# Kernel optimization log

Hardware: AMD Instinct MI355X
Metric: run time of the kernel (lower is better)

Reference implementation:

```python
import jax, jax.numpy as jnp
import numpy as np

H = 32  # GRU hidden size fixed by the module


def setup_inputs() -> dict:
    key = jax.random.key(0)
    ks = jax.random.split(key, 6)
    B, T, F = 4096, 60, 158
    s_ih = 1.0 / np.sqrt(H)
    return {
        "x": jax.random.normal(ks[0], (B, T, F), dtype=jnp.float32),
        "w_ih": jax.random.normal(ks[1], (3 * H, F), dtype=jnp.float32) * s_ih,
        "w_hh": jax.random.normal(ks[2], (3 * H, H), dtype=jnp.float32) * s_ih,
        "w1": jax.random.normal(ks[3], (16, H), dtype=jnp.float32) * (1.0 / np.sqrt(H)),
        "b1": jax.random.normal(ks[4], (16,), dtype=jnp.float32) * 0.01,
        "w2": jax.random.normal(ks[5], (1, 16), dtype=jnp.float32) * 0.25,
    }


def _gru_last_hidden(x, w_ih, w_hh):
    # x: [B, T, F]. Precompute input projections for all timesteps (one big GEMM),
    # then scan the sequential hidden-state recurrence over T.
    B = x.shape[0]
    gi = jnp.einsum("btf,gf->tbg", x, w_ih)  # [T, B, 3H]
    h0 = jnp.zeros((B, H), dtype=x.dtype)

    def step(h, gi_t):
        gh = h @ w_hh.T  # [B, 3H]
        i_r, i_z, i_n = jnp.split(gi_t, 3, axis=-1)
        h_r, h_z, h_n = jnp.split(gh, 3, axis=-1)
        r = jax.nn.sigmoid(i_r + h_r)
        z = jax.nn.sigmoid(i_z + h_z)
        n = jnp.tanh(i_n + r * h_n)
        h_new = (1.0 - z) * n + z * h
        return h_new, None

    h_last, _ = jax.lax.scan(step, h0, gi)
    return h_last  # [B, H]


def reference(x, w_ih, w_hh, w1, b1, w2):
    h = _gru_last_hidden(x, w_ih, w_hh)          # h_n[-1]: [B, 32]
    y = jax.nn.relu(h @ w1.T + b1)               # [B, 16]
    return y @ w2.T                              # [B, 1]
```

## Files before the change

### kernel.cpp

```cpp
#include <hip/hip_runtime.h>
#include <hip/hip_bf16.h>

#define BATCH 4096
#define TT 60
#define FF 158
#define HH 32
#define GG 96

typedef float f4 __attribute__((ext_vector_type(4), aligned(4)));
typedef float f2 __attribute__((ext_vector_type(2), aligned(4)));

__device__ __forceinline__ float fexp(float x) {
    return __builtin_amdgcn_exp2f(x * 1.442695040888963f);
}
__device__ __forceinline__ float fsigmoid(float x) {
    return __builtin_amdgcn_rcpf(1.0f + fexp(-x));
}
__device__ __forceinline__ float ftanh(float x) {
    float e = fexp(2.0f * x);
    return (e - 1.0f) * __builtin_amdgcn_rcpf(e + 1.0f);
}

__global__ __launch_bounds__(256, 2) void k1_gemm(
    const float* __restrict__ x, const float* __restrict__ w_ih,
    float* __restrict__ gs, int t0, int Tc)
{
    __shared__ float wsT[GG][161];
    __shared__ float xs[4][8][132];

    const int tid  = threadIdx.x;
    const int lane = tid & 63;
    const int wv   = tid >> 6;

    for (int i = tid; i < GG * FF; i += 256) {
        int g = i / FF;
        int k = i - g * FF;
        wsT[g][k] = w_ih[i];
    }

    const int tcol = lane & 15;
    const int trow = lane >> 4;
    const int g0   = tcol * 6;

    const int srow = lane >> 1;
    const int q    = lane & 1;
    const int Rs   = blockIdx.x * 128 + wv * 32 + srow;
    const int bs   = Rs / Tc;
    const int ts   = Rs - bs * Tc;
    const float* xrow = x + ((size_t)bs * TT + (size_t)(t0 + ts)) * FF + q * 4;

    {
        f4 p0 = *(const f4*)xrow;
        xs[wv][q * 4 + 0][srow] = p0.x;
        xs[wv][q * 4 + 1][srow] = p0.y;
        xs[wv][q * 4 + 2][srow] = p0.z;
        xs[wv][q * 4 + 3][srow] = p0.w;
    }
    __syncthreads();

    float acc[8][6];
    #pragma unroll
    for (int u = 0; u < 8; ++u)
        #pragma unroll
        for (int i = 0; i < 6; ++i) acc[u][i] = 0.0f;

    for (int s = 0; s < 19; ++s) {
        const int  k0n  = (s + 1) * 8;
        const bool tnxt = (s == 18);
        f4 pfn; f2 pf2;
        if (!tnxt) {
            pfn = *(const f4*)(xrow + k0n);
        } else {
            if (q == 0) pfn = *(const f4*)(xrow + k0n);
            else        pf2 = *(const f2*)(xrow + k0n);
        }

        const int kbase = s * 8;
        #pragma unroll
        for (int kk = 0; kk < 8; ++kk) {
            const f4 a0 = *(const f4*)&xs[wv][kk][trow * 8];
            const f4 a1 = *(const f4*)&xs[wv][kk][trow * 8 + 4];
            float bv[6];
            #pragma unroll
            for (int i = 0; i < 6; ++i) bv[i] = wsT[g0 + i][kbase + kk];
            #pragma unroll
            for (int i = 0; i < 6; ++i) {
                acc[0][i] = fmaf(a0.x, bv[i], acc[0][i]);
                acc[1][i] = fmaf(a0.y, bv[i], acc[1][i]);
                acc[2][i] = fmaf(a0.z, bv[i], acc[2][i]);
                acc[3][i] = fmaf(a0.w, bv[i], acc[3][i]);
                acc[4][i] = fmaf(a1.x, bv[i], acc[4][i]);
                acc[5][i] = fmaf(a1.y, bv[i], acc[5][i]);
                acc[6][i] = fmaf(a1.z, bv[i], acc[6][i]);
                acc[7][i] = fmaf(a1.w, bv[i], acc[7][i]);
            }
        }

        if (!tnxt) {
            xs[wv][q * 4 + 0][srow] = pfn.x;
            xs[wv][q * 4 + 1][srow] = pfn.y;
            xs[wv][q * 4 + 2][srow] = pfn.z;
            xs[wv][q * 4 + 3][srow] = pfn.w;
        } else {
            if (q == 0) {
                xs[wv][0][srow] = pfn.x;
                xs[wv][1][srow] = pfn.y;
                xs[wv][2][srow] = pfn.z;
                xs[wv][3][srow] = pfn.w;
            } else {
                xs[wv][4][srow] = pf2.x;
                xs[wv][5][srow] = pf2.y;
            }
        }
    }
    {
        #pragma unroll
        for (int kk = 0; kk < 6; ++kk) {
            const f4 a0 = *(const f4*)&xs[wv][kk][trow * 8];
            const f4 a1 = *(const f4*)&xs[wv][kk][trow * 8 + 4];
            float bv[6];
            #pragma unroll
            for (int i = 0; i < 6; ++i) bv[i] = wsT[g0 + i][152 + kk];
            #pragma unroll
            for (int i = 0; i < 6; ++i) {
                acc[0][i] = fmaf(a0.x, bv[i], acc[0][i]);
                acc[1][i] = fmaf(a0.y, bv[i], acc[1][i]);
                acc[2][i] = fmaf(a0.z, bv[i], acc[2][i]);
                acc[3][i] = fmaf(a0.w, bv[i], acc[3][i]);
                acc[4][i] = fmaf(a1.x, bv[i], acc[4][i]);
                acc[5][i] = fmaf(a1.y, bv[i], acc[5][i]);
                acc[6][i] = fmaf(a1.z, bv[i], acc[6][i]);
                acc[7][i] = fmaf(a1.w, bv[i], acc[7][i]);
            }
        }
    }

    #pragma unroll
    for (int u = 0; u < 8; ++u) {
        int R2 = blockIdx.x * 128 + wv * 32 + trow * 8 + u;
        int b2 = R2 / Tc;
        int t2 = R2 - b2 * Tc;
        float* dst = gs + ((size_t)t2 * BATCH + b2) * GG + g0;
        f2 v0 = {acc[u][0], acc[u][1]};
        f2 v1 = {acc[u][2], acc[u][3]};
        f2 v2 = {acc[u][4], acc[u][5]};
        *(f2*)(dst)     = v0;
        *(f2*)(dst + 2) = v1;
        *(f2*)(dst + 4) = v2;
    }
}

__global__ __launch_bounds__(256, 2) void k2_rec(
    const float* __restrict__ gs, const float* __restrict__ w_hh,
    float* __restrict__ hio, int Tc, int first, int last,
    const float* __restrict__ w1, const float* __restrict__ b1,
    const float* __restrict__ w2, float* __restrict__ out)
{
    __shared__ float hs[8][36];
    __shared__ float ys[8][16];
    const int tid = threadIdx.x;
    const int bl  = tid >> 5;
    const int j   = tid & 31;
    const int b   = blockIdx.x * 8 + bl;

    float wr[32], wz[32], wn[32];
    #pragma unroll
    for (int kk = 0; kk < 8; ++kk) {
        f4 a = *(const f4*)&w_hh[(size_t)(j     ) * HH + kk * 4];
        f4 c = *(const f4*)&w_hh[(size_t)(j + 32) * HH + kk * 4];
        f4 d = *(const f4*)&w_hh[(size_t)(j + 64) * HH + kk * 4];
        wr[kk*4] = a.x; wr[kk*4+1] = a.y; wr[kk*4+2] = a.z; wr[kk*4+3] = a.w;
        wz[kk*4] = c.x; wz[kk*4+1] = c.y; wz[kk*4+2] = c.z; wz[kk*4+3] = c.w;
        wn[kk*4] = d.x; wn[kk*4+1] = d.y; wn[kk*4+2] = d.z; wn[kk*4+3] = d.w;
    }

    float h = first ? 0.0f : hio[(size_t)b * HH + j];
    hs[bl][j] = h;

    const float*  gb = gs + (size_t)b * GG + j;
    const size_t  TS = (size_t)BATCH * GG;

#define K2_STEP(GIR, GIZ, GIN) {                                              \
        float gr = 0.0f, gz = 0.0f, gn = 0.0f;                                \
        _Pragma("unroll")                                                     \
        for (int k = 0; k < 32; k += 4) {                                     \
            f4 hv = *(const f4*)&hs[bl][k];                                   \
            gr = fmaf(wr[k  ], hv.x, gr); gz = fmaf(wz[k  ], hv.x, gz); gn = fmaf(wn[k  ], hv.x, gn); \
            gr = fmaf(wr[k+1], hv.y, gr); gz = fmaf(wz[k+1], hv.y, gz); gn = fmaf(wn[k+1], hv.y, gn); \
            gr = fmaf(wr[k+2], hv.z, gr); gz = fmaf(wz[k+2], hv.z, gz); gn = fmaf(wn[k+2], hv.z, gn); \
            gr = fmaf(wr[k+3], hv.w, gr); gz = fmaf(wz[k+3], hv.w, gz); gn = fmaf(wn[k+3], hv.w, gn); \
        }                                                                     \
        float r = fsigmoid((GIR) + gr);                                       \
        float z = fsigmoid((GIZ) + gz);                                       \
        float n = ftanh((GIN) + r * gn);                                      \
        h = (1.0f - z) * n + z * h;                                           \
        hs[bl][j] = h;                                                        \
    }

    float c0[18], c1[18];
    const int nfull = Tc / 6;

    if (nfull > 0) {
        #pragma unroll
        for (int u = 0; u < 6; ++u) {
            c0[u*3+0] = gb[(size_t)u * TS];
            c0[u*3+1] = gb[(size_t)u * TS + 32];
            c0[u*3+2] = gb[(size_t)u * TS + 64];
        }
    }

    int c = 0;
    while (c < nfull) {
        if (c + 1 < nfull) {
            const int tb = (c + 1) * 6;
            #pragma unroll
            for (int u = 0; u < 6; ++u) {
                c1[u*3+0] = gb[(size_t)(tb+u) * TS];
                c1[u*3+1] = gb[(size_t)(tb+u) * TS + 32];
                c1[u*3+2] = gb[(size_t)(tb+u) * TS + 64];
            }
        }
        #pragma unroll
        for (int u = 0; u < 6; ++u) K2_STEP(c0[u*3], c0[u*3+1], c0[u*3+2]);
        ++c;
        if (c >= nfull) break;

        if (c + 1 < nfull) {
            const int tb = (c + 1) * 6;
            #pragma unroll
            for (int u = 0; u < 6; ++u) {
                c0[u*3+0] = gb[(size_t)(tb+u) * TS];
                c0[u*3+1] = gb[(size_t)(tb+u) * TS + 32];
                c0[u*3+2] = gb[(size_t)(tb+u) * TS + 64];
            }
        }
        #pragma unroll
        for (int u = 0; u < 6; ++u) K2_STEP(c1[u*3], c1[u*3+1], c1[u*3+2]);
        ++c;
    }
    for (int t = nfull * 6; t < Tc; ++t) {
        float gir = gb[(size_t)t * TS];
        float giz = gb[(size_t)t * TS + 32];
        float gin = gb[(size_t)t * TS + 64];
        K2_STEP(gir, giz, gin);
    }
#undef K2_STEP

    if (last) {
        if (j < 16) {
            float y = b1[j];
            #pragma unroll
            for (int k = 0; k < 32; ++k) y = fmaf(w1[j * HH + k], hs[bl][k], y);
            ys[bl][j] = fmaxf(y, 0.0f);
        }
        if (j == 0) {
            float o = 0.0f;
            #pragma unroll
            for (int k = 0; k < 16; ++k) o = fmaf(ys[bl][k], w2[k], o);
            out[b] = o;
        }
    } else {
        hio[(size_t)b * HH + j] = h;
    }
}

extern "C" void kernel_launch(void* const* d_in, const int* in_sizes, int n_in,
                              void* d_out, int out_size, void* d_ws, size_t ws_size,
                              hipStream_t stream)
{
    const float* x    = (const float*)d_in[0];
    const float* w_ih = (const float*)d_in[1];
    const float* w_hh = (const float*)d_in[2];
    const float* w1   = (const float*)d_in[3];
    const float* b1   = (const float*)d_in[4];
    const float* w2   = (const float*)d_in[5];
    float* out = (float*)d_out;

    const size_t hbytes = (size_t)BATCH * HH * 4;
    size_t avail = (ws_size > hbytes) ? (ws_size - hbytes) : 0;
    int Tc = (int)(avail / ((size_t)BATCH * GG * 4));
    if (Tc > TT) Tc = TT;
    if (Tc < 1) Tc = 1;

    float* gsbuf = (float*)d_ws;
    float* hio   = (float*)((char*)d_ws + (size_t)BATCH * GG * 4 * (size_t)Tc);

    for (int t0 = 0; t0 < TT; ) {
        int tc = TT - t0; if (tc > Tc) tc = Tc;
        k1_gemm<<<BATCH * tc / 128, 256, 0, stream>>>(x, w_ih, gsbuf, t0, tc);
        int first = (t0 == 0) ? 1 : 0;
        int lastf = (t0 + tc >= TT) ? 1 : 0;
        k2_rec<<<BATCH / 8, 256, 0, stream>>>(gsbuf, w_hh, hio, tc, first, lastf,
                                              w1, b1, w2, out);
        t0 += tc;
    }
}
```

Before: 329.5 us.

## Halve k1 LDS footprint via two-phase weight staging; split k2 dot-product chains

Result: slower. 429.3 us (+30.3%).

```diff
diff --git a/kernel.cpp b/kernel.cpp
--- a/kernel.cpp
+++ b/kernel.cpp
@@ -21,22 +21,16 @@
     return (e - 1.0f) * __builtin_amdgcn_rcpf(e + 1.0f);
 }
 
-__global__ __launch_bounds__(256, 2) void k1_gemm(
+__global__ __launch_bounds__(256, 4) void k1_gemm(
     const float* __restrict__ x, const float* __restrict__ w_ih,
     float* __restrict__ gs, int t0, int Tc)
 {
-    __shared__ float wsT[GG][161];
-    __shared__ float xs[4][8][132];
+    __shared__ float ws[80][97];
+    __shared__ float xs[4][8][32];
 
     const int tid  = threadIdx.x;
     const int lane = tid & 63;
     const int wv   = tid >> 6;
-
-    for (int i = tid; i < GG * FF; i += 256) {
-        int g = i / FF;
-        int k = i - g * FF;
-        wsT[g][k] = w_ih[i];
-    }
 
     const int tcol = lane & 15;
     const int trow = lane >> 4;
@@ -49,6 +43,11 @@
     const int ts   = Rs - bs * Tc;
     const float* xrow = x + ((size_t)bs * TT + (size_t)(t0 + ts)) * FF + q * 4;
 
+    for (int i = tid; i < GG * 80; i += 256) {
+        int g = i / 80;
+        int k = i - g * 80;
+        ws[k][g] = w_ih[g * FF + k];
+    }
     {
         f4 p0 = *(const f4*)xrow;
         xs[wv][q * 4 + 0][srow] = p0.x;
@@ -64,43 +63,63 @@
         #pragma unroll
         for (int i = 0; i < 6; ++i) acc[u][i] = 0.0f;
 
-    for (int s = 0; s < 19; ++s) {
-        const int  k0n  = (s + 1) * 8;
-        const bool tnxt = (s == 18);
+#define K1_INNER(KL) {                                                        \
+        const f4 a0 = *(const f4*)&xs[wv][kk][trow * 8];                      \
+        const f4 a1 = *(const f4*)&xs[wv][kk][trow * 8 + 4];                  \
+        const f2 b01 = *(const f2*)&ws[KL][g0];                               \
+        const f2 b23 = *(const f2*)&ws[KL][g0 + 2];                           \
+        const f2 b45 = *(const f2*)&ws[KL][g0 + 4];                           \
+        const float bv[6] = {b01.x, b01.y, b23.x, b23.y, b45.x, b45.y};       \
+        _Pragma("unroll")                                                     \
+        for (int i = 0; i < 6; ++i) {                                         \
+            acc[0][i] = fmaf(a0.x, bv[i], acc[0][i]);                         \
+            acc[1][i] = fmaf(a0.y, bv[i], acc[1][i]);                         \
+            acc[2][i] = fmaf(a0.z, bv[i], acc[2][i]);                         \
+            acc[3][i] = fmaf(a0.w, bv[i], acc[3][i]);                         \
+            acc[4][i] = fmaf(a1.x, bv[i], acc[4][i]);                         \
+            acc[5][i] = fmaf(a1.y, bv[i], acc[5][i]);                         \
+            acc[6][i] = fmaf(a1.z, bv[i], acc[6][i]);                         \
+            acc[7][i] = fmaf(a1.w, bv[i], acc[7][i]);                         \
+        }                                                                     \
+    }
+
+#define K1_STAGE_F4(P) {                                                      \
+        xs[wv][q * 4 + 0][srow] = (P).x;                                      \
+        xs[wv][q * 4 + 1][srow] = (P).y;                                      \
+        xs[wv][q * 4 + 2][srow] = (P).z;                                      \
+        xs[wv][q * 4 + 3][srow] = (P).w;                                      \
+    }
+
+    for (int s = 0; s < 10; ++s) {
+        f4 pfn = *(const f4*)(xrow + (s + 1) * 8);
+        const int kb = s * 8;
+        #pragma unroll
+        for (int kk = 0; kk < 8; ++kk) K1_INNER(kb + kk)
+        K1_STAGE_F4(pfn)
+    }
+
+    __syncthreads();
+    for (int i = tid; i < GG * 78; i += 256) {
+        int g = i / 78;
+        int k = i - g * 78;
+        ws[k][g] = w_ih[g * FF + 80 + k];
+    }
+    __syncthreads();
+
+    for (int s = 0; s < 9; ++s) {
+        const int k0n = 88 + s * 8;
         f4 pfn; f2 pf2;
-        if (!tnxt) {
+        if (s < 8) {
             pfn = *(const f4*)(xrow + k0n);
         } else {
-            if (q == 0) pfn = *(const f4*)(xrow + k0n);
-            else        pf2 = *(const f2*)(xrow + k0n);
-        }
-
-        const int kbase = s * 8;
+            if (q == 0) pfn = *(const f4*)(xrow + 152);
+            else        pf2 = *(const f2*)(xrow + 152);
+        }
+        const int kb = s * 8;
         #pragma unroll
-        for (int kk = 0; kk < 8; ++kk) {
-            const f4 a0 = *(const f4*)&xs[wv][kk][trow * 8];
-            const f4 a1 = *(const f4*)&xs[wv][kk][trow * 8 + 4];
-            float bv[6];
-            #pragma unroll
-            for (int i = 0; i < 6; ++i) bv[i] = wsT[g0 + i][kbase + kk];
-            #pragma unroll
-            for (int i = 0; i < 6; ++i) {
-                acc[0][i] = fmaf(a0.x, bv[i], acc[0][i]);
-                acc[1][i] = fmaf(a0.y, bv[i], acc[1][i]);
-                acc[2][i] = fmaf(a0.z, bv[i], acc[2][i]);
-                acc[3][i] = fmaf(a0.w, bv[i], acc[3][i]);
-                acc[4][i] = fmaf(a1.x, bv[i], acc[4][i]);
-                acc[5][i] = fmaf(a1.y, bv[i], acc[5][i]);
-                acc[6][i] = fmaf(a1.z, bv[i], acc[6][i]);
-                acc[7][i] = fmaf(a1.w, bv[i], acc[7][i]);
-            }
-        }
-
-        if (!tnxt) {
-            xs[wv][q * 4 + 0][srow] = pfn.x;
-            xs[wv][q * 4 + 1][srow] = pfn.y;
-            xs[wv][q * 4 + 2][srow] = pfn.z;
-            xs[wv][q * 4 + 3][srow] = pfn.w;
+        for (int kk = 0; kk < 8; ++kk) K1_INNER(kb + kk)
+        if (s < 8) {
+            K1_STAGE_F4(pfn)
         } else {
             if (q == 0) {
                 xs[wv][0][srow] = pfn.x;
@@ -113,27 +132,11 @@
             }
         }
     }
-    {
-        #pragma unroll
-        for (int kk = 0; kk < 6; ++kk) {
-            const f4 a0 = *(const f4*)&xs[wv][kk][trow * 8];
-            const f4 a1 = *(const f4*)&xs[wv][kk][trow * 8 + 4];
-            float bv[6];
-            #pragma unroll
-            for (int i = 0; i < 6; ++i) bv[i] = wsT[g0 + i][152 + kk];
-            #pragma unroll
-            for (int i = 0; i < 6; ++i) {
-                acc[0][i] = fmaf(a0.x, bv[i], acc[0][i]);
-                acc[1][i] = fmaf(a0.y, bv[i], acc[1][i]);
-                acc[2][i] = fmaf(a0.z, bv[i], acc[2][i]);
-                acc[3][i] = fmaf(a0.w, bv[i], acc[3][i]);
-                acc[4][i] = fmaf(a1.x, bv[i], acc[4][i]);
-                acc[5][i] = fmaf(a1.y, bv[i], acc[5][i]);
-                acc[6][i] = fmaf(a1.z, bv[i], acc[6][i]);
-                acc[7][i] = fmaf(a1.w, bv[i], acc[7][i]);
-            }
-        }
-    }
+    #pragma unroll
+    for (int kk = 0; kk < 6; ++kk) K1_INNER(72 + kk)
+
+#undef K1_INNER
+#undef K1_STAGE_F4
 
     #pragma unroll
     for (int u = 0; u < 8; ++u) {
@@ -181,70 +184,66 @@
     const size_t  TS = (size_t)BATCH * GG;
 
 #define K2_STEP(GIR, GIZ, GIN) {                                              \
-        float gr = 0.0f, gz = 0.0f, gn = 0.0f;                                \
-        _Pragma("unroll")                                                     \
-        for (int k = 0; k < 32; k += 4) {                                     \
+        float gr0 = 0.f, gz0 = 0.f, gn0 = 0.f;                                \
+        float gr1 = 0.f, gz1 = 0.f, gn1 = 0.f;                                \
+        _Pragma("unroll")                                                     \
+        for (int k = 0; k < 16; k += 4) {                                     \
             f4 hv = *(const f4*)&hs[bl][k];                                   \
-            gr = fmaf(wr[k  ], hv.x, gr); gz = fmaf(wz[k  ], hv.x, gz); gn = fmaf(wn[k  ], hv.x, gn); \
-            gr = fmaf(wr[k+1], hv.y, gr); gz = fmaf(wz[k+1], hv.y, gz); gn = fmaf(wn[k+1], hv.y, gn); \
-            gr = fmaf(wr[k+2], hv.z, gr); gz = fmaf(wz[k+2], hv.z, gz); gn = fmaf(wn[k+2], hv.z, gn); \
-            gr = fmaf(wr[k+3], hv.w, gr); gz = fmaf(wz[k+3], hv.w, gz); gn = fmaf(wn[k+3], hv.w, gn); \
-        }                                                                     \
-        float r = fsigmoid((GIR) + gr);                                       \
-        float z = fsigmoid((GIZ) + gz);                                       \
-        float n = ftanh((GIN) + r * gn);                                      \
+            gr0 = fmaf(wr[k  ], hv.x, gr0); gz0 = fmaf(wz[k  ], hv.x, gz0); gn0 = fmaf(wn[k  ], hv.x, gn0); \
+            gr0 = fmaf(wr[k+1], hv.y, gr0); gz0 = fmaf(wz[k+1], hv.y, gz0); gn0 = fmaf(wn[k+1], hv.y, gn0); \
+            gr0 = fmaf(wr[k+2], hv.z, gr0); gz0 = fmaf(wz[k+2], hv.z, gz0); gn0 = fmaf(wn[k+2], hv.z, gn0); \
+            gr0 = fmaf(wr[k+3], hv.w, gr0); gz0 = fmaf(wz[k+3], hv.w, gz0); gn0 = fmaf(wn[k+3], hv.w, gn0); \
+        }                                                                     \
+        _Pragma("unroll")                                                     \
+        for (int k = 16; k < 32; k += 4) {                                    \
+            f4 hv = *(const f4*)&hs[bl][k];                                   \
+            gr1 = fmaf(wr[k  ], hv.x, gr1); gz1 = fmaf(wz[k  ], hv.x, gz1); gn1 = fmaf(wn[k  ], hv.x, gn1); \
+            gr1 = fmaf(wr[k+1], hv.y, gr1); gz1 = fmaf(wz[k+1], hv.y, gz1); gn1 = fmaf(wn[k+1], hv.y, gn1); \
+            gr1 = fmaf(wr[k+2], hv.z, gr1); gz1 = fmaf(wz[k+2], hv.z, gz1); gn1 = fmaf(wn[k+2], hv.z, gn1); \
+            gr1 = fmaf(wr[k+3], hv.w, gr1); gz1 = fmaf(wz[k+3], hv.w, gz1); gn1 = fmaf(wn[k+3], hv.w, gn1); \
+        }                                                                     \
+        float r = fsigmoid((GIR) + gr0 + gr1);                                \
+        float z = fsigmoid((GIZ) + gz0 + gz1);                                \
+        float n = ftanh((GIN) + r * (gn0 + gn1));                             \
         h = (1.0f - z) * n + z * h;                                           \
         hs[bl][j] = h;                                                        \
     }
 
-    float c0[18], c1[18];
-    const int nfull = Tc / 6;
-
-    if (nfull > 0) {
-        #pragma unroll
-        for (int u = 0; u < 6; ++u) {
-            c0[u*3+0] = gb[(size_t)u * TS];
-            c0[u*3+1] = gb[(size_t)u * TS + 32];
-            c0[u*3+2] = gb[(size_t)u * TS + 64];
-        }
-    }
-
-    int c = 0;
-    while (c < nfull) {
-        if (c + 1 < nfull) {
-            const int tb = (c + 1) * 6;
-            #pragma unroll
-            for (int u = 0; u < 6; ++u) {
-                c1[u*3+0] = gb[(size_t)(tb+u) * TS];
-                c1[u*3+1] = gb[(size_t)(tb+u) * TS + 32];
-                c1[u*3+2] = gb[(size_t)(tb+u) * TS + 64];
-            }
-        }
-        #pragma unroll
-        for (int u = 0; u < 6; ++u) K2_STEP(c0[u*3], c0[u*3+1], c0[u*3+2]);
-        ++c;
-        if (c >= nfull) break;
-
-        if (c + 1 < nfull) {
-            const int tb = (c + 1) * 6;
-            #pragma unroll
-            for (int u = 0; u < 6; ++u) {
-                c0[u*3+0] = gb[(size_t)(tb+u) * TS];
-                c0[u*3+1] = gb[(size_t)(tb+u) * TS + 32];
-                c0[u*3+2] = gb[(size_t)(tb+u) * TS + 64];
-            }
-        }
-        #pragma unroll
-        for (int u = 0; u < 6; ++u) K2_STEP(c1[u*3], c1[u*3+1], c1[u*3+2]);
-        ++c;
-    }
-    for (int t = nfull * 6; t < Tc; ++t) {
-        float gir = gb[(size_t)t * TS];
-        float giz = gb[(size_t)t * TS + 32];
-        float gin = gb[(size_t)t * TS + 64];
-        K2_STEP(gir, giz, gin);
+#define K2_LOAD6(DST, TBASE) {                                                \
+        _Pragma("unroll")                                                     \
+        for (int u = 0; u < 6; ++u) {                                         \
+            DST[u*3+0] = gb[(size_t)((TBASE) + u) * TS];                      \
+            DST[u*3+1] = gb[(size_t)((TBASE) + u) * TS + 32];                 \
+            DST[u*3+2] = gb[(size_t)((TBASE) + u) * TS + 64];                 \
+        }                                                                     \
+    }
+
+#define K2_RUN6(SRC) {                                                        \
+        _Pragma("unroll")                                                     \
+        for (int u = 0; u < 6; ++u) K2_STEP(SRC[u*3], SRC[u*3+1], SRC[u*3+2]) \
+    }
+
+    if (Tc == 60) {
+        float c0[18], c1[18];
+        K2_LOAD6(c0, 0)
+        #pragma unroll 1
+        for (int p = 0; p < 5; ++p) {
+            K2_LOAD6(c1, p * 12 + 6)
+            K2_RUN6(c0)
+            if (p < 4) K2_LOAD6(c0, p * 12 + 12)
+            K2_RUN6(c1)
+        }
+    } else {
+        for (int t = 0; t < Tc; ++t) {
+            float gir = gb[(size_t)t * TS];
+            float giz = gb[(size_t)t * TS + 32];
+            float gin = gb[(size_t)t * TS + 64];
+            K2_STEP(gir, giz, gin)
+        }
     }
 #undef K2_STEP
+#undef K2_LOAD6
+#undef K2_RUN6
 
     if (last) {
         if (j < 16) {
```
